# Kernel optimization log

Measured on AMD Instinct MI355X. Metric: run time of the kernel, lower is better.

Reference implementation:

```python
import jax, jax.numpy as jnp
import numpy as np

B, L, K, D = 4, 2048, 100000, 64


def setup_inputs() -> dict:
    key = jax.random.key(0)
    k1, k2, k3, k4 = jax.random.split(key, 4)
    identities = jax.random.randint(k1, (B, L), 0, K)
    # raw times in [0, 10000], sorted per sequence (event times are increasing)
    times = jnp.sort(jax.random.uniform(k2, (B, L), jnp.float32, 0.0, 10000.0), axis=-1)
    mask = jnp.ones((B, 1, L), jnp.float32)
    # learned parameters (padding_idx=0 rows zeroed, as in nn.Embedding(..., 0))
    emb = (jax.random.normal(k3, (K, D), jnp.float32) * 0.02).at[0].set(0.0)
    u_table = (jax.random.normal(k4, (K,), jnp.float32) * 0.1).at[0].set(0.0)
    beta = jnp.array([0.1], jnp.float32)
    return {"identities": identities, "times": times, "mask": mask,
            "emb": emb, "u_table": u_table, "beta": beta}


def reference(identities, times, mask, emb, u_table, beta):
    t = times / 10000.0                       # (B, L)
    ab = jnp.abs(beta)[0]                     # scalar |beta|
    # time_difference[b,i,j] = t[b,i] - t[b,j]
    td = t[:, :, None] - t[:, None, :]        # (B, L, L)
    weighted_exp = ab * jnp.exp(-ab * td)     # (B, L, L)
    e = emb[identities]                       # (B, L, D)
    alpha = jnp.einsum('bid,bjd->bij', e, e)  # (B, L, L)
    u_k = jnp.abs(u_table[identities])        # (B, L)
    # sum_time_difference[b,i,j] = t[b,-1] - t[b,j]  (independent of i)
    std = t[:, -1, None] - t                  # (B, L)
    horizon = (t[:, -1] - t[:, 1])[:, None]   # (B, 1)
    negative_integral = -u_k * horizon - jnp.einsum(
        'bij,bj->bi', alpha, 1.0 - jnp.exp(-ab * std))   # (B, L)
    before_sum = jnp.tril(alpha * weighted_exp, k=-1)    # (B, L, L)
    mask_sum = before_sum * mask                         # (B, L, L)
    lam = jnp.abs(mask_sum.sum(-1) + u_k) + 1e-6         # (B, L)
    log_lambda = -jnp.log(lam) - negative_integral       # (B, L)
    return log_lambda.sum(-1)                            # (B,)
```

## Files before the change

### kernel.cpp

```cpp
#include <hip/hip_runtime.h>


#define BB 4
#define LL 2048
#define DD 64
#define CL 64
#define NC (LL / CL)

#define LOADF(p)     __hip_atomic_load((p), __ATOMIC_RELAXED, __HIP_MEMORY_SCOPE_AGENT)
#define STOREF(p, v) __hip_atomic_store((p), (v), __ATOMIC_RELAXED, __HIP_MEMORY_SCOPE_AGENT)

__global__ __launch_bounds__(64) void fused_hawkes(
    const int* __restrict__ ids, const float* __restrict__ times,
    const float* __restrict__ mask, const float* __restrict__ emb,
    const float* __restrict__ u_table, const float* __restrict__ beta,
    float* __restrict__ S, float* __restrict__ Ep, float* __restrict__ Vp,
    float* __restrict__ Ctr, int* __restrict__ flag1, int* __restrict__ flag2,
    float* __restrict__ out)
{
    __shared__ float E [CL][DD + 1];
    __shared__ float LP[CL][DD + 1];
    __shared__ float wm[CL];

    const int blk = blockIdx.x;
    const int b = blk / NC, c = blk % NC;
    const int lane = threadIdx.x;
    const int j0 = c * CL;
    const int rec = b * NC + c;

    const float ab = fabsf(beta[0]);
    const float tl = times[b * LL + LL - 1] * 1e-4f;
    const float t1 = times[b * LL + 1] * 1e-4f;
    const float horizon = tl - t1;
    const float ce = expf(-ab * tl);

    const int   myid = ids  [b * LL + j0 + lane];
    const float myt  = times[b * LL + j0 + lane] * 1e-4f;
    const float mym  = mask [b * LL + j0 + lane];
    const float myuk = fabsf(u_table[myid]);

    wm[lane] = expf(ab * myt) * mym;

    float s = 0.f, ep = 0.f, vp = 0.f;
#pragma unroll 16
    for (int jj = 0; jj < CL; ++jj) {
        const int   id = __shfl(myid, jj);
        const float t  = __shfl(myt,  jj);
        const float m  = __shfl(mym,  jj);
        const float e  = emb[(long)id * DD + lane];
        const float w  = expf(ab * t);
        E[jj][lane] = e;
        s  += e * w * m;
        ep += e;
        vp += e * (1.f - ce * w);
    }

    STOREF(&S [rec * DD + lane], s);
    STOREF(&Ep[rec * DD + lane], ep);
    STOREF(&Vp[rec * DD + lane], vp);
    __threadfence();
    if (lane == 0)
        __hip_atomic_store(&flag1[rec], 1, __ATOMIC_RELEASE, __HIP_MEMORY_SCOPE_AGENT);

    for (int cc = 0; cc < c; ++cc)
        while (__hip_atomic_load(&flag1[b * NC + cc], __ATOMIC_ACQUIRE,
                                 __HIP_MEMORY_SCOPE_AGENT) != 1)
            __builtin_amdgcn_s_sleep(1);

    float run = 0.f;
#pragma unroll 8
    for (int cc = 0; cc < c; ++cc)
        run += LOADF(&S[(b * NC + cc) * DD + lane]);

    __syncthreads();

#pragma unroll 8
    for (int i = 0; i < CL; ++i) {
        LP[i][lane] = run;
        run += E[i][lane] * wm[i];
    }
    __syncthreads();

    float acc = 0.f;
#pragma unroll
    for (int k = 0; k < DD; ++k)
        acc += E[lane][k] * LP[lane][k];

    const float s1  = ab * expf(-ab * myt) * acc;
    const float lam = fabsf(s1 + myuk) + 1e-6f;
    const float rowContrib = -logf(lam) + myuk * horizon;

    if (c != NC - 1) {
        float v = rowContrib;
#pragma unroll
        for (int off = 32; off > 0; off >>= 1)
            v += __shfl_xor(v, off);
        if (lane == 0) {
            STOREF(&Ctr[rec], v);
            __threadfence();
            __hip_atomic_store(&flag2[rec], 1, __ATOMIC_RELEASE, __HIP_MEMORY_SCOPE_AGENT);
        }
    } else {
        for (int cc = 0; cc < NC - 1; ++cc)
            while (__hip_atomic_load(&flag2[b * NC + cc], __ATOMIC_ACQUIRE,
                                     __HIP_MEMORY_SCOPE_AGENT) != 1)
                __builtin_amdgcn_s_sleep(1);

        float et = 0.f, vt = 0.f;
#pragma unroll 8
        for (int cc = 0; cc < NC; ++cc) {
            et += LOADF(&Ep[(b * NC + cc) * DD + lane]);
            vt += LOADF(&Vp[(b * NC + cc) * DD + lane]);
        }
        float oc = (lane < NC - 1) ? LOADF(&Ctr[b * NC + lane]) : 0.f;

        float v = rowContrib + et * vt + oc;
#pragma unroll
        for (int off = 32; off > 0; off >>= 1)
            v += __shfl_xor(v, off);
        if (lane == 0)
            out[b] = v;
    }
}

extern "C" void kernel_launch(void* const* d_in, const int* in_sizes, int n_in,
                              void* d_out, int out_size, void* d_ws, size_t ws_size,
                              hipStream_t stream)
{
    const int*   ids     = (const int*)  d_in[0];
    const float* times   = (const float*)d_in[1];
    const float* mask    = (const float*)d_in[2];
    const float* emb     = (const float*)d_in[3];
    const float* u_table = (const float*)d_in[4];
    const float* beta    = (const float*)d_in[5];
    float* outp = (float*)d_out;

    float* ws    = (float*)d_ws;
    float* S     = ws;
    float* Ep    = S   + BB * NC * DD;
    float* Vp    = Ep  + BB * NC * DD;
    float* Ctr   = Vp  + BB * NC * DD;
    int*   flag1 = (int*)(Ctr + BB * NC);
    int*   flag2 = flag1 + BB * NC;

    fused_hawkes<<<BB * NC, 64, 0, stream>>>(ids, times, mask, emb, u_table,
                                             beta, S, Ep, Vp, Ctr,
                                             flag1, flag2, outp);
}
```

Before: 117.1 us.

## Halve chunk size and replace shared-memory row dot products with wave shuffle reductions

Chunk length drops from 64 to 32, which doubles the number of blocks so the embedding gathers are spread across more CUs. Each block now keeps its gathered embedding rows in registers instead of shared memory. It computes each row's intensity dot product with a running prefix and a cross-lane shuffle reduction, which removes the shared-memory tiles and barriers. The cost is a longer serial prefix chain (more chunk records each block must wait for and sum). There are also 32 sequential wave reductions per block, and higher register pressure from the unrolled 32-element array.

```diff
diff --git a/kernel.cpp b/kernel.cpp
--- a/kernel.cpp
+++ b/kernel.cpp
@@ -4,7 +4,7 @@
 #define BB 4
 #define LL 2048
 #define DD 64
-#define CL 64
+#define CL 32
 #define NC (LL / CL)
 
 #define LOADF(p)     __hip_atomic_load((p), __ATOMIC_RELAXED, __HIP_MEMORY_SCOPE_AGENT)
@@ -18,13 +18,10 @@
     float* __restrict__ Ctr, int* __restrict__ flag1, int* __restrict__ flag2,
     float* __restrict__ out)
 {
-    __shared__ float E [CL][DD + 1];
-    __shared__ float LP[CL][DD + 1];
-    __shared__ float wm[CL];
-
     const int blk = blockIdx.x;
     const int b = blk / NC, c = blk % NC;
     const int lane = threadIdx.x;
+    const int row  = lane & (CL - 1);
     const int j0 = c * CL;
     const int rec = b * NC + c;
 
@@ -34,25 +31,28 @@
     const float horizon = tl - t1;
     const float ce = expf(-ab * tl);
 
-    const int   myid = ids  [b * LL + j0 + lane];
-    const float myt  = times[b * LL + j0 + lane] * 1e-4f;
-    const float mym  = mask [b * LL + j0 + lane];
+    const int   myid = ids  [b * LL + j0 + row];
+    const float myt  = times[b * LL + j0 + row] * 1e-4f;
+    const float mym  = mask [b * LL + j0 + row];
     const float myuk = fabsf(u_table[myid]);
+    const float wlane  = expf(ab * myt);
+    const float wmlane = wlane * mym;
 
-    wm[lane] = expf(ab * myt) * mym;
+    float e[CL];
+#pragma unroll
+    for (int j = 0; j < CL; ++j) {
+        const int id = __shfl(myid, j);
+        e[j] = emb[(long)id * DD + lane];
+    }
 
     float s = 0.f, ep = 0.f, vp = 0.f;
-#pragma unroll 16
-    for (int jj = 0; jj < CL; ++jj) {
-        const int   id = __shfl(myid, jj);
-        const float t  = __shfl(myt,  jj);
-        const float m  = __shfl(mym,  jj);
-        const float e  = emb[(long)id * DD + lane];
-        const float w  = expf(ab * t);
-        E[jj][lane] = e;
-        s  += e * w * m;
-        ep += e;
-        vp += e * (1.f - ce * w);
+#pragma unroll
+    for (int j = 0; j < CL; ++j) {
+        const float wm = __shfl(wmlane, j);
+        const float w  = __shfl(wlane,  j);
+        s  += e[j] * wm;
+        ep += e[j];
+        vp += e[j] * (1.f - ce * w);
     }
 
     STOREF(&S [rec * DD + lane], s);
@@ -68,35 +68,26 @@
             __builtin_amdgcn_s_sleep(1);
 
     float run = 0.f;
-#pragma unroll 8
     for (int cc = 0; cc < c; ++cc)
         run += LOADF(&S[(b * NC + cc) * DD + lane]);
 
-    __syncthreads();
-
-#pragma unroll 8
-    for (int i = 0; i < CL; ++i) {
-        LP[i][lane] = run;
-        run += E[i][lane] * wm[i];
+    float total = 0.f;
+#pragma unroll
+    for (int j = 0; j < CL; ++j) {
+        float d = e[j] * run;
+#pragma unroll
+        for (int off = 32; off > 0; off >>= 1)
+            d += __shfl_xor(d, off);
+        const float tj = __shfl(myt,  j);
+        const float uj = __shfl(myuk, j);
+        const float lam = fabsf(ab * expf(-ab * tj) * d + uj) + 1e-6f;
+        total += -logf(lam) + uj * horizon;
+        run += e[j] * __shfl(wmlane, j);
     }
-    __syncthreads();
-
-    float acc = 0.f;
-#pragma unroll
-    for (int k = 0; k < DD; ++k)
-        acc += E[lane][k] * LP[lane][k];
-
-    const float s1  = ab * expf(-ab * myt) * acc;
-    const float lam = fabsf(s1 + myuk) + 1e-6f;
-    const float rowContrib = -logf(lam) + myuk * horizon;
 
     if (c != NC - 1) {
-        float v = rowContrib;
-#pragma unroll
-        for (int off = 32; off > 0; off >>= 1)
-            v += __shfl_xor(v, off);
         if (lane == 0) {
-            STOREF(&Ctr[rec], v);
+            STOREF(&Ctr[rec], total);
             __threadfence();
             __hip_atomic_store(&flag2[rec], 1, __ATOMIC_RELEASE, __HIP_MEMORY_SCOPE_AGENT);
         }
@@ -112,14 +103,13 @@
             et += LOADF(&Ep[(b * NC + cc) * DD + lane]);
             vt += LOADF(&Vp[(b * NC + cc) * DD + lane]);
         }
-        float oc = (lane < NC - 1) ? LOADF(&Ctr[b * NC + lane]) : 0.f;
-
-        float v = rowContrib + et * vt + oc;
+        float v = et * vt;
+        if (lane < NC - 1) v += LOADF(&Ctr[b * NC + lane]);
 #pragma unroll
         for (int off = 32; off > 0; off >>= 1)
             v += __shfl_xor(v, off);
         if (lane == 0)
-            out[b] = v;
+            out[b] = v + total;
     }
 }
 
```

Measured after the change: 184.3 us. 57.4% more time.

## Split fused flag-synchronized kernel into three sequential launches

Applied to the files above, without the earlier changes.

Replaces the single kernel that used global flags and spin-waits between blocks with three launches: per-chunk sums, a per-chunk scan and dot, and a final reduction. The launches themselves act as the barriers, so the atomic flag polling and fences go away. The negative-integral term is distributed per chunk as Ep_c·Vtotal instead of being done in the last block. The cost is two extra launch overheads, and the embedding rows are gathered twice, once in k1 and again in k2.

```diff
diff --git a/kernel.cpp b/kernel.cpp
--- a/kernel.cpp
+++ b/kernel.cpp
@@ -7,16 +7,50 @@
 #define CL 64
 #define NC (LL / CL)
 
-#define LOADF(p)     __hip_atomic_load((p), __ATOMIC_RELAXED, __HIP_MEMORY_SCOPE_AGENT)
-#define STOREF(p, v) __hip_atomic_store((p), (v), __ATOMIC_RELAXED, __HIP_MEMORY_SCOPE_AGENT)
+__global__ __launch_bounds__(64) void k1_sums(
+    const int* __restrict__ ids, const float* __restrict__ times,
+    const float* __restrict__ mask, const float* __restrict__ emb,
+    const float* __restrict__ beta,
+    float* __restrict__ S, float* __restrict__ Ep, float* __restrict__ Vp)
+{
+    const int blk = blockIdx.x;
+    const int b = blk / NC, c = blk % NC;
+    const int lane = threadIdx.x;
+    const int j0 = c * CL;
+    const int rec = b * NC + c;
 
-__global__ __launch_bounds__(64) void fused_hawkes(
+    const float ab = fabsf(beta[0]);
+    const float tl = times[b * LL + LL - 1] * 1e-4f;
+    const float ce = expf(-ab * tl);
+
+    const int   myid = ids  [b * LL + j0 + lane];
+    const float myt  = times[b * LL + j0 + lane] * 1e-4f;
+    const float mym  = mask [b * LL + j0 + lane];
+    const float wlane  = expf(ab * myt);
+    const float wmlane = wlane * mym;
+
+    float s = 0.f, ep = 0.f, vp = 0.f;
+#pragma unroll 16
+    for (int jj = 0; jj < CL; ++jj) {
+        const int   id = __shfl(myid, jj);
+        const float w  = __shfl(wlane,  jj);
+        const float wm = __shfl(wmlane, jj);
+        const float e  = emb[(long)id * DD + lane];
+        s  += e * wm;
+        ep += e;
+        vp += e * (1.f - ce * w);
+    }
+    S [rec * DD + lane] = s;
+    Ep[rec * DD + lane] = ep;
+    Vp[rec * DD + lane] = vp;
+}
+
+__global__ __launch_bounds__(64) void k2_scan(
     const int* __restrict__ ids, const float* __restrict__ times,
     const float* __restrict__ mask, const float* __restrict__ emb,
     const float* __restrict__ u_table, const float* __restrict__ beta,
-    float* __restrict__ S, float* __restrict__ Ep, float* __restrict__ Vp,
-    float* __restrict__ Ctr, int* __restrict__ flag1, int* __restrict__ flag2,
-    float* __restrict__ out)
+    const float* __restrict__ S, const float* __restrict__ Ep,
+    const float* __restrict__ Vp, float* __restrict__ Ctr)
 {
     __shared__ float E [CL][DD + 1];
     __shared__ float LP[CL][DD + 1];
@@ -32,46 +66,27 @@
     const float tl = times[b * LL + LL - 1] * 1e-4f;
     const float t1 = times[b * LL + 1] * 1e-4f;
     const float horizon = tl - t1;
-    const float ce = expf(-ab * tl);
 
     const int   myid = ids  [b * LL + j0 + lane];
     const float myt  = times[b * LL + j0 + lane] * 1e-4f;
     const float mym  = mask [b * LL + j0 + lane];
     const float myuk = fabsf(u_table[myid]);
-
     wm[lane] = expf(ab * myt) * mym;
 
-    float s = 0.f, ep = 0.f, vp = 0.f;
+    float vt = 0.f;
+#pragma unroll 8
+    for (int cc = 0; cc < NC; ++cc)
+        vt += Vp[(b * NC + cc) * DD + lane];
+    float run = 0.f;
+    for (int cc = 0; cc < c; ++cc)
+        run += S[(b * NC + cc) * DD + lane];
+    const float epc = Ep[rec * DD + lane];
+
 #pragma unroll 16
     for (int jj = 0; jj < CL; ++jj) {
-        const int   id = __shfl(myid, jj);
-        const float t  = __shfl(myt,  jj);
-        const float m  = __shfl(mym,  jj);
-        const float e  = emb[(long)id * DD + lane];
-        const float w  = expf(ab * t);
-        E[jj][lane] = e;
-        s  += e * w * m;
-        ep += e;
-        vp += e * (1.f - ce * w);
+        const int id = __shfl(myid, jj);
+        E[jj][lane] = emb[(long)id * DD + lane];
     }
-
-    STOREF(&S [rec * DD + lane], s);
-    STOREF(&Ep[rec * DD + lane], ep);
-    STOREF(&Vp[rec * DD + lane], vp);
-    __threadfence();
-    if (lane == 0)
-        __hip_atomic_store(&flag1[rec], 1, __ATOMIC_RELEASE, __HIP_MEMORY_SCOPE_AGENT);
-
-    for (int cc = 0; cc < c; ++cc)
-        while (__hip_atomic_load(&flag1[b * NC + cc], __ATOMIC_ACQUIRE,
-                                 __HIP_MEMORY_SCOPE_AGENT) != 1)
-            __builtin_amdgcn_s_sleep(1);
-
-    float run = 0.f;
-#pragma unroll 8
-    for (int cc = 0; cc < c; ++cc)
-        run += LOADF(&S[(b * NC + cc) * DD + lane]);
-
     __syncthreads();
 
 #pragma unroll 8
@@ -86,41 +101,26 @@
     for (int k = 0; k < DD; ++k)
         acc += E[lane][k] * LP[lane][k];
 
-    const float s1  = ab * expf(-ab * myt) * acc;
-    const float lam = fabsf(s1 + myuk) + 1e-6f;
-    const float rowContrib = -logf(lam) + myuk * horizon;
+    const float lam = fabsf(ab * expf(-ab * myt) * acc + myuk) + 1e-6f;
+    float v = -logf(lam) + myuk * horizon + epc * vt;
+#pragma unroll
+    for (int off = 32; off > 0; off >>= 1)
+        v += __shfl_xor(v, off);
+    if (lane == 0)
+        Ctr[rec] = v;
+}
 
-    if (c != NC - 1) {
-        float v = rowContrib;
+__global__ __launch_bounds__(64) void k3_final(
+    const float* __restrict__ Ctr, float* __restrict__ out)
+{
+    const int b = blockIdx.x;
+    const int lane = threadIdx.x;
+    float v = (lane < NC) ? Ctr[b * NC + lane] : 0.f;
 #pragma unroll
-        for (int off = 32; off > 0; off >>= 1)
-            v += __shfl_xor(v, off);
-        if (lane == 0) {
-            STOREF(&Ctr[rec], v);
-            __threadfence();
-            __hip_atomic_store(&flag2[rec], 1, __ATOMIC_RELEASE, __HIP_MEMORY_SCOPE_AGENT);
-        }
-    } else {
-        for (int cc = 0; cc < NC - 1; ++cc)
-            while (__hip_atomic_load(&flag2[b * NC + cc], __ATOMIC_ACQUIRE,
-                                     __HIP_MEMORY_SCOPE_AGENT) != 1)
-                __builtin_amdgcn_s_sleep(1);
-
-        float et = 0.f, vt = 0.f;
-#pragma unroll 8
-        for (int cc = 0; cc < NC; ++cc) {
-            et += LOADF(&Ep[(b * NC + cc) * DD + lane]);
-            vt += LOADF(&Vp[(b * NC + cc) * DD + lane]);
-        }
-        float oc = (lane < NC - 1) ? LOADF(&Ctr[b * NC + lane]) : 0.f;
-
-        float v = rowContrib + et * vt + oc;
-#pragma unroll
-        for (int off = 32; off > 0; off >>= 1)
-            v += __shfl_xor(v, off);
-        if (lane == 0)
-            out[b] = v;
-    }
+    for (int off = 32; off > 0; off >>= 1)
+        v += __shfl_xor(v, off);
+    if (lane == 0)
+        out[b] = v;
 }
 
 extern "C" void kernel_launch(void* const* d_in, const int* in_sizes, int n_in,
@@ -135,15 +135,14 @@
     const float* beta    = (const float*)d_in[5];
     float* outp = (float*)d_out;
 
-    float* ws    = (float*)d_ws;
-    float* S     = ws;
-    float* Ep    = S   + BB * NC * DD;
-    float* Vp    = Ep  + BB * NC * DD;
-    float* Ctr   = Vp  + BB * NC * DD;
-    int*   flag1 = (int*)(Ctr + BB * NC);
-    int*   flag2 = flag1 + BB * NC;
+    float* ws  = (float*)d_ws;
+    float* S   = ws;
+    float* Ep  = S  + BB * NC * DD;
+    float* Vp  = Ep + BB * NC * DD;
+    float* Ctr = Vp + BB * NC * DD;
 
-    fused_hawkes<<<BB * NC, 64, 0, stream>>>(ids, times, mask, emb, u_table,
-                                             beta, S, Ep, Vp, Ctr,
-                                             flag1, flag2, outp);
+    k1_sums<<<BB * NC, 64, 0, stream>>>(ids, times, mask, emb, beta, S, Ep, Vp);
+    k2_scan<<<BB * NC, 64, 0, stream>>>(ids, times, mask, emb, u_table, beta,
+                                        S, Ep, Vp, Ctr);
+    k3_final<<<BB, 64, 0, stream>>>(Ctr, outp);
 }
```

Result: faster. 96.05 us (-18.0%).
